# Performance work log

Measured on AMD Instinct MI355X. Metric: run time of the kernel, lower is better.

## Reference

```python
import jax, jax.numpy as jnp
import numpy as np

L, D, H, EXP = 4, 512, 8, 4
HD = D // H
DFF = D * EXP
B, S = 8, 1024
LN_EPS = 1e-3  # keras LayerNormalization default epsilon


def _glorot(key, shape):
    fan_in, fan_out = shape[-2], shape[-1]
    lim = np.sqrt(6.0 / (fan_in + fan_out))
    return jax.random.uniform(key, shape, jnp.float32, -lim, lim)


def setup_inputs() -> dict:
    key = jax.random.key(0)
    ks = jax.random.split(key, 12)
    x = jax.random.normal(ks[0], (B, S, D), jnp.float32)
    # sequence mask from random lengths (mimics tf.sequence_mask(row_lengths))
    lengths = jax.random.randint(ks[1], (B,), S // 2, S + 1)
    mask = (jnp.arange(S)[None, :] < lengths[:, None])  # [B,S] bool
    inp = {
        'x': x, 'mask': mask,
        'Wq': _glorot(ks[2], (L, D, D)),
        'Wk': _glorot(ks[3], (L, D, D)),
        'Wv': _glorot(ks[4], (L, D, D)),
        'Wo': _glorot(ks[5], (L, D, D)),
        'ln1_g': jnp.ones((L, D), jnp.float32),
        'ln1_b': jnp.zeros((L, D), jnp.float32),
        'ln2_g': jnp.ones((L, D), jnp.float32),
        'ln2_b': jnp.zeros((L, D), jnp.float32),
        'W1': _glorot(ks[6], (L, D, DFF)),
        'b1': jnp.zeros((L, DFF), jnp.float32),
        'W2': _glorot(ks[7], (L, DFF, D)),
        'b2': jnp.zeros((L, D), jnp.float32),
    }
    return inp


def _layernorm(x, g, b):
    mu = jnp.mean(x, axis=-1, keepdims=True)
    var = jnp.mean(jnp.square(x - mu), axis=-1, keepdims=True)
    return (x - mu) * jax.lax.rsqrt(var + LN_EPS) * g + b


def _pos_encoding(s, d):
    # matches the source: sin/cos halves with inv freq 10000**(2j/d), j<d/2
    half = d // 2
    p = jnp.arange(s, dtype=jnp.float32)[:, None]          # [S,1]
    inv = 10000.0 ** (2.0 * jnp.arange(half, dtype=jnp.float32) / d)  # [half]
    ang = p / inv[None, :]                                 # [S,half]
    return jnp.concatenate([jnp.sin(ang), jnp.cos(ang)], axis=1)  # [S,D]


def _forward(x, mask, Wq, Wk, Wv, Wo, ln1_g, ln1_b, ln2_g, ln2_b, W1, b1, W2, b2):
    b, s, d = x.shape
    x = x + _pos_encoding(s, d)
    key_mask = mask[:, None, None, :]  # [B,1,1,Sk]
    scale = 1.0 / jnp.sqrt(jnp.float32(HD))
    for l in range(L):
        h = _layernorm(x, ln1_g[l], ln1_b[l])
        q = (h @ Wq[l]).reshape(b, s, H, HD).transpose(0, 2, 1, 3)  # bhsd
        k = (h @ Wk[l]).reshape(b, s, H, HD).transpose(0, 2, 1, 3)
        v = (h @ Wv[l]).reshape(b, s, H, HD).transpose(0, 2, 1, 3)
        scores = jnp.einsum('bhqd,bhkd->bhqk', q, k) * scale
        scores = jnp.where(key_mask, scores, -1e9)
        attn = jax.nn.softmax(scores, axis=-1)
        o = jnp.einsum('bhqk,bhkd->bhqd', attn, v)
        o = o.transpose(0, 2, 1, 3).reshape(b, s, d) @ Wo[l]
        x = x + o  # dropout rate 0 / inference -> identity
        h = _layernorm(x, ln2_g[l], ln2_b[l])
        f = jax.nn.relu(h @ W1[l] + b1[l]) @ W2[l] + b2[l]
        x = x + f
    return x


def reference(x, mask, Wq, Wk, Wv, Wo, ln1_g, ln1_b, ln2_g, ln2_b, W1, b1, W2, b2):
    return _forward(x, mask, Wq, Wk, Wv, Wo, ln1_g, ln1_b, ln2_g, ln2_b, W1, b1, W2, b2)
```

## Files before the change

### kernel.cpp

```cpp
#include <hip/hip_runtime.h>
#include <math.h>

#define NB 8
#define SEQ 1024
#define DM 512
#define NH 8
#define HDIM 64
#define DFF 2048
#define NLAYER 4
#define NTOK (NB * SEQ)
#define QKVD 1536

typedef __attribute__((ext_vector_type(8))) short bf16x8;
typedef __attribute__((ext_vector_type(4))) float f32x4;

__device__ __forceinline__ ushort f2bf(float f) {
    union { float f; unsigned u; } v; v.f = f;
    unsigned r = (v.u + 0x7FFF + ((v.u >> 16) & 1)) >> 16;
    return (ushort)r;
}

__device__ __forceinline__ void async16(const void* g, void* l) {
    __builtin_amdgcn_global_load_lds(
        (const __attribute__((address_space(1))) unsigned int*)g,
        (__attribute__((address_space(3))) unsigned int*)l, 16, 0, 0);
}

__global__ __launch_bounds__(256) void add_pos_kernel(const float* __restrict__ x,
                                                      float* __restrict__ out) {
    int idx4 = blockIdx.x * blockDim.x + threadIdx.x;
    int base = idx4 * 4;
    int d = base & (DM - 1);
    int s = (base >> 9) & (SEQ - 1);
    float4 v = *(const float4*)&x[base];
    float r[4] = {v.x, v.y, v.z, v.w};
#pragma unroll
    for (int i = 0; i < 4; i++) {
        int dd = d + i;
        float pe;
        if (dd < 256) {
            float inv = powf(10000.0f, 2.0f * (float)dd / 512.0f);
            pe = sinf((float)s / inv);
        } else {
            float inv = powf(10000.0f, 2.0f * (float)(dd - 256) / 512.0f);
            pe = cosf((float)s / inv);
        }
        r[i] += pe;
    }
    *(float4*)&out[base] = make_float4(r[0], r[1], r[2], r[3]);
}

__global__ __launch_bounds__(256) void wtrans_kernel(const float* __restrict__ src,
                                                     ushort* __restrict__ dst,
                                                     int K, int N, int rowOff,
                                                     int layerStride) {
    __shared__ float tile[32][36];
    int l = blockIdx.z;
    int kb = blockIdx.y * 32, nb = blockIdx.x * 32;
    const float* s = src + (size_t)l * K * N;
    ushort* d = dst + (size_t)l * layerStride;
    int r = threadIdx.x >> 3, c4 = (threadIdx.x & 7) * 4;
    float4 v = *(const float4*)&s[(size_t)(kb + r) * N + nb + c4];
    *(float4*)&tile[r][c4] = v;
    __syncthreads();
    ushort4 o;
    o.x = f2bf(tile[c4 + 0][r]);
    o.y = f2bf(tile[c4 + 1][r]);
    o.z = f2bf(tile[c4 + 2][r]);
    o.w = f2bf(tile[c4 + 3][r]);
    *(ushort4*)&d[(size_t)(rowOff + nb + r) * K + kb + c4] = o;
}

__global__ __launch_bounds__(256) void ln_kernel(const float* __restrict__ x,
                                                 const float* __restrict__ g,
                                                 const float* __restrict__ bta,
                                                 ushort* __restrict__ out) {
    int w = threadIdx.x >> 6;
    int lane = threadIdx.x & 63;
    size_t row = (size_t)blockIdx.x * 4 + w;
    const float* xr = x + row * DM;
    float4 v0 = *(const float4*)&xr[lane * 4];
    float4 v1 = *(const float4*)&xr[256 + lane * 4];
    float sum = v0.x + v0.y + v0.z + v0.w + v1.x + v1.y + v1.z + v1.w;
#pragma unroll
    for (int off = 32; off > 0; off >>= 1) sum += __shfl_xor(sum, off, 64);
    float mu = sum * (1.0f / 512.0f);
    float d0[8] = {v0.x - mu, v0.y - mu, v0.z - mu, v0.w - mu,
                   v1.x - mu, v1.y - mu, v1.z - mu, v1.w - mu};
    float sq = 0.0f;
#pragma unroll
    for (int i = 0; i < 8; i++) sq = fmaf(d0[i], d0[i], sq);
#pragma unroll
    for (int off = 32; off > 0; off >>= 1) sq += __shfl_xor(sq, off, 64);
    float rs = rsqrtf(sq * (1.0f / 512.0f) + 1e-3f);
    float4 g0 = *(const float4*)&g[lane * 4];
    float4 g1 = *(const float4*)&g[256 + lane * 4];
    float4 b0 = *(const float4*)&bta[lane * 4];
    float4 b1 = *(const float4*)&bta[256 + lane * 4];
    ushort* orow = out + row * DM;
    ushort4 o0, o1;
    o0.x = f2bf(fmaf(d0[0] * rs, g0.x, b0.x));
    o0.y = f2bf(fmaf(d0[1] * rs, g0.y, b0.y));
    o0.z = f2bf(fmaf(d0[2] * rs, g0.z, b0.z));
    o0.w = f2bf(fmaf(d0[3] * rs, g0.w, b0.w));
    o1.x = f2bf(fmaf(d0[4] * rs, g1.x, b1.x));
    o1.y = f2bf(fmaf(d0[5] * rs, g1.y, b1.y));
    o1.z = f2bf(fmaf(d0[6] * rs, g1.z, b1.z));
    o1.w = f2bf(fmaf(d0[7] * rs, g1.w, b1.w));
    *(ushort4*)&orow[lane * 4] = o0;
    *(ushort4*)&orow[256 + lane * 4] = o1;
}

template <int BM, int BN, int KH, int MODE>
__global__ __launch_bounds__(256) void gemm_bf16(const ushort* __restrict__ A,
                                                 const ushort* __restrict__ Bt,
                                                 const float* __restrict__ bias,
                                                 void* __restrict__ Cv,
                                                 void* __restrict__ aux,
                                                 int M, int N, int K) {
    static_assert(BM % 64 == 0 && BN % 64 == 0, "tile multiple of 64");
    constexpr int FM = BM / 32;
    constexpr int FN = BN / 32;
    __shared__ __align__(16) ushort As[2][KH * BM * 32];
    __shared__ __align__(16) ushort Bs[2][KH * BN * 32];
    const int tid = threadIdx.x;
    const int lane = tid & 63;
    const int w = tid >> 6;

    const int nx = gridDim.x;
    int wg = blockIdx.y * nx + blockIdx.x;
    int xcd = wg & 7;
    int t0 = wg >> 3;
    int bx = t0 % nx;
    int by = (t0 / nx) * 8 + xcd;
    const int m0 = by * BM, n0 = bx * BN;

    const int wm = (w >> 1) * (BM / 2), wn = (w & 1) * (BN / 2);
    const int fm = lane & 15, fq = lane >> 4;

    f32x4 acc[FM][FN] = {};

    auto stage = [&](int buf, int kt) {
#pragma unroll
        for (int hf = 0; hf < KH; hf++) {
#pragma unroll
            for (int u = 0; u < BM / 64; u++) {
                int chunk = u * 256 + tid;
                int row = chunk >> 2, c = chunk & 3;
                async16(&A[(size_t)(m0 + row) * K + kt + hf * 32 + c * 8],
                        (char*)As[buf] + hf * BM * 64 + chunk * 16);
            }
#pragma unroll
            for (int u = 0; u < BN / 64; u++) {
                int chunk = u * 256 + tid;
                int row = chunk >> 2, c = chunk & 3;
                async16(&Bt[(size_t)(n0 + row) * K + kt + hf * 32 + c * 8],
                        (char*)Bs[buf] + hf * BN * 64 + chunk * 16);
            }
        }
    };

    stage(0, 0);
    __syncthreads();
    int cur = 0;
    for (int kt = 0; kt < K; kt += 32 * KH) {
        if (kt + 32 * KH < K) stage(cur ^ 1, kt + 32 * KH);
#pragma unroll
        for (int hf = 0; hf < KH; hf++) {
            bf16x8 af[FM], bfr[FN];
#pragma unroll
            for (int i = 0; i < FM; i++)
                af[i] = *(const bf16x8*)&As[cur][hf * BM * 32 +
                                                 (wm + i * 16 + fm) * 32 + fq * 8];
#pragma unroll
            for (int j = 0; j < FN; j++)
                bfr[j] = *(const bf16x8*)&Bs[cur][hf * BN * 32 +
                                                  (wn + j * 16 + fm) * 32 + fq * 8];
#pragma unroll
            for (int i = 0; i < FM; i++)
#pragma unroll
                for (int j = 0; j < FN; j++)
                    acc[i][j] = __builtin_amdgcn_mfma_f32_16x16x32_bf16(
                        af[i], bfr[j], acc[i][j], 0, 0, 0);
        }
        __syncthreads();
        cur ^= 1;
    }

    if constexpr (MODE == 5) {
        if (n0 >= 1024) {
            ushort* vT = (ushort*)aux;
            const int b = m0 >> 10;
            const int sl = (m0 & (SEQ - 1)) + wm + fq * 4;
#pragma unroll
            for (int i = 0; i < FM; i++) {
#pragma unroll
                for (int j = 0; j < FN; j++) {
                    int c = n0 - 1024 + wn + j * 16 + fm;
                    ushort4 o;
                    o.x = f2bf(acc[i][j][0]);
                    o.y = f2bf(acc[i][j][1]);
                    o.z = f2bf(acc[i][j][2]);
                    o.w = f2bf(acc[i][j][3]);
                    *(ushort4*)&vT[(size_t)(b * DM + c) * SEQ + sl + i * 16] = o;
                }
            }
        } else {
#pragma unroll
            for (int i = 0; i < FM; i++)
#pragma unroll
                for (int j = 0; j < FN; j++) {
                    int col = n0 + wn + j * 16 + fm;
#pragma unroll
                    for (int r = 0; r < 4; r++) {
                        int row = m0 + wm + i * 16 + fq * 4 + r;
                        ((ushort*)Cv)[(size_t)row * N + col] = f2bf(acc[i][j][r]);
                    }
                }
        }
        return;
    }

#pragma unroll
    for (int i = 0; i < FM; i++) {
#pragma unroll
        for (int j = 0; j < FN; j++) {
            int col = n0 + wn + j * 16 + fm;
#pragma unroll
            for (int r = 0; r < 4; r++) {
                int row = m0 + wm + i * 16 + fq * 4 + r;
                float vv = acc[i][j][r];
                if constexpr (MODE == 0) {
                    ((ushort*)Cv)[(size_t)row * N + col] = f2bf(vv);
                } else if constexpr (MODE == 1) {
                    float* C = (float*)Cv;
                    C[(size_t)row * N + col] += vv;
                } else if constexpr (MODE == 2) {
                    vv += bias[col];
                    vv = fmaxf(vv, 0.0f);
                    ((ushort*)Cv)[(size_t)row * N + col] = f2bf(vv);
                } else {
                    float* C = (float*)Cv;
                    C[(size_t)row * N + col] += vv + bias[col];
                }
            }
        }
    }
}

__global__ __launch_bounds__(256) void attn_mfma(const ushort* __restrict__ QKV,
                                                 const ushort* __restrict__ Vt,
                                                 const int* __restrict__ mask,
                                                 ushort* __restrict__ O) {
    __shared__ __align__(16) ushort Kt[64 * 64];
    __shared__ __align__(16) ushort Vs[64 * 64];
    __shared__ __align__(16) ushort ps[4][16 * 72];
    __shared__ float mskf[64];
    __shared__ int lensh[4];

    const int tid = threadIdx.x, lane = tid & 63, w = tid >> 6;
    const int h = blockIdx.y, b = blockIdx.z;
    const int q0 = blockIdx.x * 64 + w * 16;
    const int fm = lane & 15, fq = lane >> 4;
    ushort* pw = &ps[w][0];
    const float L2E = 1.44269504f;

    int part = mask[b * SEQ + tid] + mask[b * SEQ + 256 + tid] +
               mask[b * SEQ + 512 + tid] + mask[b * SEQ + 768 + tid];
#pragma unroll
    for (int off = 32; off > 0; off >>= 1) part += __shfl_xor(part, off, 64);
    if (lane == 0) lensh[w] = part;

    bf16x8 qf[2];
#pragma unroll
    for (int kk = 0; kk < 2; kk++) {
        bf16x8 t = *(const bf16x8*)&QKV[(size_t)(b * SEQ + q0 + fm) * QKVD + h * HDIM +
                                        kk * 32 + fq * 8];
#pragma unroll
        for (int j = 0; j < 8; j++) {
            union { float f; unsigned u; } vv;
            vv.u = ((unsigned)(ushort)t[j]) << 16;
            vv.f *= 0.125f;
            t[j] = (short)(ushort)(vv.u >> 16);
        }
        qf[kk] = t;
    }

    const int r0 = tid >> 3, c0 = tid & 7;
    const int r1 = r0 + 32;
    const int dk0 = (r0 * 8 + (c0 ^ (r0 & 7))) * 16;
    const int dk1 = (r1 * 8 + (c0 ^ (r1 & 7))) * 16;

    auto gK = [&](int j0, int rr) {
        return (const uint4*)&QKV[(size_t)(b * SEQ + j0 + rr) * QKVD + 512 +
                                  h * HDIM + c0 * 8];
    };
    auto gV = [&](int j0, int rr) {
        return (const uint4*)&Vt[(size_t)((b * NH + h) * HDIM + rr) * SEQ + j0 + c0 * 8];
    };

    uint4 kreg0 = *gK(0, r0), kreg1 = *gK(0, r1);
    uint4 vreg0 = *gV(0, r0), vreg1 = *gV(0, r1);
    int mreg = (tid < 64) ? mask[b * SEQ + tid] : 0;
    *(uint4*)((char*)Kt + dk0) = kreg0;
    *(uint4*)((char*)Kt + dk1) = kreg1;
    *(uint4*)((char*)Vs + dk0) = vreg0;
    *(uint4*)((char*)Vs + dk1) = vreg1;
    if (tid < 64) mskf[tid] = mreg ? 1.0f : 0.0f;
    __syncthreads();

    const int len = lensh[0] + lensh[1] + lensh[2] + lensh[3];
    const int jmax = (len + 63) & ~63;

    f32x4 oacc[4] = {};
    float mrow = -INFINITY, lrow = 0.0f;

    for (int j0 = 0; j0 < jmax; j0 += 64) {
        const bool has_next = (j0 + 64 < jmax);
        if (has_next) {
            kreg0 = *gK(j0 + 64, r0);
            kreg1 = *gK(j0 + 64, r1);
            vreg0 = *gV(j0 + 64, r0);
            vreg1 = *gV(j0 + 64, r1);
            if (tid < 64) mreg = mask[b * SEQ + j0 + 64 + tid];
        }

        f32x4 sc[4] = {};
        __builtin_amdgcn_s_setprio(1);
#pragma unroll
        for (int nt = 0; nt < 4; nt++) {
            int key = nt * 16 + fm;
#pragma unroll
            for (int kk = 0; kk < 2; kk++) {
                bf16x8 kf = *(const bf16x8*)((char*)Kt +
                            (key * 8 + ((kk * 4 + fq) ^ (key & 7))) * 16);
                sc[nt] = __builtin_amdgcn_mfma_f32_16x16x32_bf16(kf, qf[kk], sc[nt], 0, 0, 0);
            }
        }
        __builtin_amdgcn_s_setprio(0);

        float mx = -INFINITY;
#pragma unroll
        for (int nt = 0; nt < 4; nt++)
#pragma unroll
            for (int r = 0; r < 4; r++) mx = fmaxf(mx, sc[nt][r]);
        mx = fmaxf(mx, __shfl_xor(mx, 16));
        mx = fmaxf(mx, __shfl_xor(mx, 32));
        if (!__all(mx - mrow <= 8.0f)) {
            float mn = fmaxf(mrow, mx);
            float alpha = __expf(mrow - mn);
            mrow = mn;
            lrow *= alpha;
#pragma unroll
            for (int nt = 0; nt < 4; nt++)
#pragma unroll
                for (int r = 0; r < 4; r++) oacc[nt][r] *= alpha;
        }

        const float nm2 = -mrow * L2E;
        const bool full = (j0 + 64 <= len);
        float sv[4][4];
        float ls = 0.0f;
        if (full) {
#pragma unroll
            for (int nt = 0; nt < 4; nt++)
#pragma unroll
                for (int r = 0; r < 4; r++) {
                    float p = exp2f(fmaf(sc[nt][r], L2E, nm2));
                    sv[nt][r] = p;
                    ls += p;
                }
        } else {
#pragma unroll
            for (int nt = 0; nt < 4; nt++) {
                f32x4 mv = *(const f32x4*)&mskf[nt * 16 + fq * 4];
#pragma unroll
                for (int r = 0; r < 4; r++) {
                    float p = exp2f(fmaf(sc[nt][r], L2E, nm2)) * mv[r];
                    sv[nt][r] = p;
                    ls += p;
                }
            }
        }
        ls += __shfl_xor(ls, 16);
        ls += __shfl_xor(ls, 32);
        lrow += ls;

#pragma unroll
        for (int nt = 0; nt < 4; nt++) {
            union { float f; unsigned u; } a0, a1, a2, a3;
            a0.f = sv[nt][0]; a1.f = sv[nt][1]; a2.f = sv[nt][2]; a3.f = sv[nt][3];
            unsigned d0 = (a0.u >> 16) | (a1.u & 0xFFFF0000u);
            unsigned d1 = (a2.u >> 16) | (a3.u & 0xFFFF0000u);
            *(uint2*)&pw[fm * 72 + nt * 16 + fq * 4] = make_uint2(d0, d1);
        }

        __builtin_amdgcn_s_setprio(1);
#pragma unroll
        for (int kk = 0; kk < 2; kk++) {
            bf16x8 pf = *(const bf16x8*)&pw[fm * 72 + kk * 32 + fq * 8];
#pragma unroll
            for (int nt = 0; nt < 4; nt++) {
                int dim = nt * 16 + fm;
                bf16x8 vf = *(const bf16x8*)((char*)Vs +
                            (dim * 8 + ((kk * 4 + fq) ^ (dim & 7))) * 16);
                oacc[nt] = __builtin_amdgcn_mfma_f32_16x16x32_bf16(vf, pf, oacc[nt], 0, 0, 0);
            }
        }
        __builtin_amdgcn_s_setprio(0);

        __syncthreads();
        if (has_next) {
            *(uint4*)((char*)Kt + dk0) = kreg0;
            *(uint4*)((char*)Kt + dk1) = kreg1;
            *(uint4*)((char*)Vs + dk0) = vreg0;
            *(uint4*)((char*)Vs + dk1) = vreg1;
            if (tid < 64) mskf[tid] = mreg ? 1.0f : 0.0f;
            __syncthreads();
        }
    }

    float inv = 1.0f / lrow;
#pragma unroll
    for (int nt = 0; nt < 4; nt++) {
        ushort4 o;
        o.x = f2bf(oacc[nt][0] * inv);
        o.y = f2bf(oacc[nt][1] * inv);
        o.z = f2bf(oacc[nt][2] * inv);
        o.w = f2bf(oacc[nt][3] * inv);
        *(ushort4*)&O[(size_t)(b * SEQ + q0 + fm) * DM + h * HDIM + nt * 16 + fq * 4] = o;
    }
}

extern "C" void kernel_launch(void* const* d_in, const int* in_sizes, int n_in,
                              void* d_out, int out_size, void* d_ws, size_t ws_size,
                              hipStream_t stream) {
    const float* x_in = (const float*)d_in[0];
    const int* mask   = (const int*)d_in[1];
    const float* Wq   = (const float*)d_in[2];
    const float* Wk   = (const float*)d_in[3];
    const float* Wv   = (const float*)d_in[4];
    const float* Wo   = (const float*)d_in[5];
    const float* ln1g = (const float*)d_in[6];
    const float* ln1b = (const float*)d_in[7];
    const float* ln2g = (const float*)d_in[8];
    const float* ln2b = (const float*)d_in[9];
    const float* W1   = (const float*)d_in[10];
    const float* b1   = (const float*)d_in[11];
    const float* W2   = (const float*)d_in[12];
    const float* b2   = (const float*)d_in[13];

    float* x = (float*)d_out;
    ushort* wsb = (ushort*)d_ws;
    const size_t U = 1048576;
    ushort* WqkvT = wsb;
    ushort* WoT   = wsb + 3 * U;
    ushort* W1T   = wsb + 4 * U;
    ushort* W2T   = wsb + 8 * U;
    ushort* hb    = wsb + 12 * U;
    ushort* qkv   = wsb + 16 * U;
    ushort* ob    = wsb + 28 * U;
    ushort* vTb   = wsb + 32 * U;
    ushort* f1b   = qkv;

    wtrans_kernel<<<dim3(16, 16, 4), 256, 0, stream>>>(Wq, WqkvT, 512, 512, 0, 786432);
    wtrans_kernel<<<dim3(16, 16, 4), 256, 0, stream>>>(Wk, WqkvT, 512, 512, 512, 786432);
    wtrans_kernel<<<dim3(16, 16, 4), 256, 0, stream>>>(Wv, WqkvT, 512, 512, 1024, 786432);
    wtrans_kernel<<<dim3(16, 16, 4), 256, 0, stream>>>(Wo, WoT, 512, 512, 0, 262144);
    wtrans_kernel<<<dim3(64, 16, 4), 256, 0, stream>>>(W1, W1T, 512, 2048, 0, 1048576);
    wtrans_kernel<<<dim3(16, 64, 4), 256, 0, stream>>>(W2, W2T, 2048, 512, 0, 1048576);

    add_pos_kernel<<<(NTOK * DM / 4) / 256, 256, 0, stream>>>(x_in, x);

    dim3 gQKV(QKVD / 64, NTOK / 128);
    dim3 gProj(DM / 64, NTOK / 64);
    dim3 gFF1(DFF / 64, NTOK / 128);
    dim3 gFF2(DM / 64, NTOK / 64);
    dim3 gAttn(SEQ / 64, NH, NB);

    for (int l = 0; l < NLAYER; l++) {
        const size_t wOff   = (size_t)l * 262144;
        const size_t wqkvOff= (size_t)l * 786432;
        const size_t w1Off  = (size_t)l * 1048576;

        ln_kernel<<<NTOK / 4, 256, 0, stream>>>(x, ln1g + l * DM, ln1b + l * DM, hb);
        gemm_bf16<128, 64, 1, 5><<<gQKV, 256, 0, stream>>>(hb, WqkvT + wqkvOff, nullptr,
                                                           qkv, vTb, NTOK, QKVD, DM);
        attn_mfma<<<gAttn, 256, 0, stream>>>(qkv, vTb, mask, ob);
        gemm_bf16<64, 64, 2, 1><<<gProj, 256, 0, stream>>>(ob, WoT + wOff, nullptr, x,
                                                           nullptr, NTOK, DM, DM);
        ln_kernel<<<NTOK / 4, 256, 0, stream>>>(x, ln2g + l * DM, ln2b + l * DM, hb);
        gemm_bf16<128, 64, 1, 2><<<gFF1, 256, 0, stream>>>(hb, W1T + w1Off,
                                                           b1 + (size_t)l * DFF, f1b,
                                                           nullptr, NTOK, DFF, DM);
        gemm_bf16<64, 64, 2, 3><<<gFF2, 256, 0, stream>>>(f1b, W2T + w1Off,
                                                          b2 + (size_t)l * DM, x,
                                                          nullptr, NTOK, DM, DFF);
    }
}
```

Before: 769.5 us.

## Double attention query tile to 128 rows with 512-thread blocks

The attention kernel now runs 8 waves per block, each handling 16 query rows, so one block covers 128 queries and every K/V tile staged in shared memory is reused by twice as many waves. Each thread now loads one K and one V row chunk per tile instead of two. The grid halves in the query dimension. The separate fast path for fully unmasked tiles is removed, so every tile multiplies by the mask, which adds a few ALU and LDS reads per tile. Fewer blocks (512) may lower occupancy balance on the GPU.

```diff
diff --git a/kernel.cpp b/kernel.cpp
--- a/kernel.cpp
+++ b/kernel.cpp
@@ -248,25 +248,24 @@
     }
 }
 
-__global__ __launch_bounds__(256) void attn_mfma(const ushort* __restrict__ QKV,
+__global__ __launch_bounds__(512) void attn_mfma(const ushort* __restrict__ QKV,
                                                  const ushort* __restrict__ Vt,
                                                  const int* __restrict__ mask,
                                                  ushort* __restrict__ O) {
     __shared__ __align__(16) ushort Kt[64 * 64];
     __shared__ __align__(16) ushort Vs[64 * 64];
-    __shared__ __align__(16) ushort ps[4][16 * 72];
+    __shared__ __align__(16) ushort ps[8][16 * 72];
     __shared__ float mskf[64];
-    __shared__ int lensh[4];
+    __shared__ int lensh[8];
 
     const int tid = threadIdx.x, lane = tid & 63, w = tid >> 6;
     const int h = blockIdx.y, b = blockIdx.z;
-    const int q0 = blockIdx.x * 64 + w * 16;
+    const int q0 = blockIdx.x * 128 + w * 16;
     const int fm = lane & 15, fq = lane >> 4;
     ushort* pw = &ps[w][0];
     const float L2E = 1.44269504f;
 
-    int part = mask[b * SEQ + tid] + mask[b * SEQ + 256 + tid] +
-               mask[b * SEQ + 512 + tid] + mask[b * SEQ + 768 + tid];
+    int part = mask[b * SEQ + tid] + mask[b * SEQ + 512 + tid];
 #pragma unroll
     for (int off = 32; off > 0; off >>= 1) part += __shfl_xor(part, off, 64);
     if (lane == 0) lensh[w] = part;
@@ -287,29 +286,26 @@
     }
 
     const int r0 = tid >> 3, c0 = tid & 7;
-    const int r1 = r0 + 32;
     const int dk0 = (r0 * 8 + (c0 ^ (r0 & 7))) * 16;
-    const int dk1 = (r1 * 8 + (c0 ^ (r1 & 7))) * 16;
-
-    auto gK = [&](int j0, int rr) {
-        return (const uint4*)&QKV[(size_t)(b * SEQ + j0 + rr) * QKVD + 512 +
+
+    auto gK = [&](int j0) {
+        return (const uint4*)&QKV[(size_t)(b * SEQ + j0 + r0) * QKVD + 512 +
                                   h * HDIM + c0 * 8];
     };
-    auto gV = [&](int j0, int rr) {
-        return (const uint4*)&Vt[(size_t)((b * NH + h) * HDIM + rr) * SEQ + j0 + c0 * 8];
+    auto gV = [&](int j0) {
+        return (const uint4*)&Vt[(size_t)((b * NH + h) * HDIM + r0) * SEQ + j0 + c0 * 8];
     };
 
-    uint4 kreg0 = *gK(0, r0), kreg1 = *gK(0, r1);
-    uint4 vreg0 = *gV(0, r0), vreg1 = *gV(0, r1);
+    uint4 kreg = *gK(0);
+    uint4 vreg = *gV(0);
     int mreg = (tid < 64) ? mask[b * SEQ + tid] : 0;
-    *(uint4*)((char*)Kt + dk0) = kreg0;
-    *(uint4*)((char*)Kt + dk1) = kreg1;
-    *(uint4*)((char*)Vs + dk0) = vreg0;
-    *(uint4*)((char*)Vs + dk1) = vreg1;
+    *(uint4*)((char*)Kt + dk0) = kreg;
+    *(uint4*)((char*)Vs + dk0) = vreg;
     if (tid < 64) mskf[tid] = mreg ? 1.0f : 0.0f;
     __syncthreads();
 
-    const int len = lensh[0] + lensh[1] + lensh[2] + lensh[3];
+    const int len = lensh[0] + lensh[1] + lensh[2] + lensh[3] +
+                    lensh[4] + lensh[5] + lensh[6] + lensh[7];
     const int jmax = (len + 63) & ~63;
 
     f32x4 oacc[4] = {};
@@ -318,10 +314,8 @@
     for (int j0 = 0; j0 < jmax; j0 += 64) {
         const bool has_next = (j0 + 64 < jmax);
         if (has_next) {
-            kreg0 = *gK(j0 + 64, r0);
-            kreg1 = *gK(j0 + 64, r1);
-            vreg0 = *gV(j0 + 64, r0);
-            vreg1 = *gV(j0 + 64, r1);
+            kreg = *gK(j0 + 64);
+            vreg = *gV(j0 + 64);
             if (tid < 64) mreg = mask[b * SEQ + j0 + 64 + tid];
         }
 
@@ -358,28 +352,16 @@
         }
 
         const float nm2 = -mrow * L2E;
-        const bool full = (j0 + 64 <= len);
         float sv[4][4];
         float ls = 0.0f;
-        if (full) {
-#pragma unroll
-            for (int nt = 0; nt < 4; nt++)
-#pragma unroll
-                for (int r = 0; r < 4; r++) {
-                    float p = exp2f(fmaf(sc[nt][r], L2E, nm2));
-                    sv[nt][r] = p;
-                    ls += p;
-                }
-        } else {
-#pragma unroll
-            for (int nt = 0; nt < 4; nt++) {
-                f32x4 mv = *(const f32x4*)&mskf[nt * 16 + fq * 4];
-#pragma unroll
-                for (int r = 0; r < 4; r++) {
-                    float p = exp2f(fmaf(sc[nt][r], L2E, nm2)) * mv[r];
-                    sv[nt][r] = p;
-                    ls += p;
-                }
+#pragma unroll
+        for (int nt = 0; nt < 4; nt++) {
+            f32x4 mv = *(const f32x4*)&mskf[nt * 16 + fq * 4];
+#pragma unroll
+            for (int r = 0; r < 4; r++) {
+                float p = exp2f(fmaf(sc[nt][r], L2E, nm2)) * mv[r];
+                sv[nt][r] = p;
+                ls += p;
             }
         }
         ls += __shfl_xor(ls, 16);
@@ -411,10 +393,8 @@
 
         __syncthreads();
         if (has_next) {
-            *(uint4*)((char*)Kt + dk0) = kreg0;
-            *(uint4*)((char*)Kt + dk1) = kreg1;
-            *(uint4*)((char*)Vs + dk0) = vreg0;
-            *(uint4*)((char*)Vs + dk1) = vreg1;
+            *(uint4*)((char*)Kt + dk0) = kreg;
+            *(uint4*)((char*)Vs + dk0) = vreg;
             if (tid < 64) mskf[tid] = mreg ? 1.0f : 0.0f;
             __syncthreads();
         }
@@ -476,7 +456,7 @@
     dim3 gProj(DM / 64, NTOK / 64);
     dim3 gFF1(DFF / 64, NTOK / 128);
     dim3 gFF2(DM / 64, NTOK / 64);
-    dim3 gAttn(SEQ / 64, NH, NB);
+    dim3 gAttn(SEQ / 128, NH, NB);
 
     for (int l = 0; l < NLAYER; l++) {
         const size_t wOff   = (size_t)l * 262144;
@@ -486,7 +466,7 @@
         ln_kernel<<<NTOK / 4, 256, 0, stream>>>(x, ln1g + l * DM, ln1b + l * DM, hb);
         gemm_bf16<128, 64, 1, 5><<<gQKV, 256, 0, stream>>>(hb, WqkvT + wqkvOff, nullptr,
                                                            qkv, vTb, NTOK, QKVD, DM);
-        attn_mfma<<<gAttn, 256, 0, stream>>>(qkv, vTb, mask, ob);
+        attn_mfma<<<gAttn, 512, 0, stream>>>(qkv, vTb, mask, ob);
         gemm_bf16<64, 64, 2, 1><<<gProj, 256, 0, stream>>>(ob, WoT + wOff, nullptr, x,
                                                            nullptr, NTOK, DM, DM);
         ln_kernel<<<NTOK / 4, 256, 0, stream>>>(x, ln2g + l * DM, ln2b + l * DM, hb);
```

After: 751.6 us. 1.02x faster.
